# Kernel optimization log

Hardware: AMD Instinct MI355X
Metric: run time of the kernel (lower is better)

Reference implementation:

```python
import jax, jax.numpy as jnp
import numpy as np

SEARCH_RANGE = 4  # matches args.search_range


def _displacements(r):
    # Exact channel ordering of the original double loop:
    # I=0 -> (0,0); then for i=1..r: (-i,0),(+i,0),(0,-i),(0,+i),
    # then for j=1..r: (-i,-j),(+i,+j),(-i,+j),(+i,-j).
    ds = [(0, 0)]
    for i in range(1, r + 1):
        ds += [(-i, 0), (i, 0), (0, -i), (0, i)]
        for j in range(1, r + 1):
            ds += [(-i, -j), (i, j), (-i, j), (i, -j)]
    return ds


def setup_inputs() -> dict:
    key = jax.random.key(0)
    k1, k2 = jax.random.split(key)
    B, C, H, W = 4, 128, 96, 160
    src = jax.random.normal(k1, (B, C, H, W), dtype=jnp.float32)
    tgt = jax.random.normal(k2, (B, C, H, W), dtype=jnp.float32)
    return {"src": src, "tgt": tgt}


def reference(src, tgt):
    r = SEARCH_RANGE
    B, C, H, W = src.shape
    D = (2 * r + 1) ** 2  # 81 displacement channels
    # Zero-pad tgt spatially so out-of-range shifted regions contribute 0,
    # matching the torch version's zero-initialized output slices.
    tgt_pad = jnp.pad(tgt, ((0, 0), (0, 0), (r, r), (r, r)))
    chans = []
    for dy, dx in _displacements(r):
        # shifted[b,c,y,x] = tgt[b,c,y+dy,x+dx] (0 outside)
        t = jax.lax.dynamic_slice(tgt_pad, (0, 0, r + dy, r + dx), (B, C, H, W))
        chans.append(jnp.einsum('bchw,bchw->bhw', src, t))
    out = jnp.stack(chans, axis=1)  # [B, D, H, W]
    return out / D
```

## Files before the change

kernel.cpp:

```cpp
#include <hip/hip_runtime.h>
#include <hip/hip_bf16.h>

#define BATCH 4
#define CHAN 128
#define HGT 96
#define WID 160
#define HW (HGT * WID)
#define THREADS 256
#define TENSOR_ELEMS (BATCH * CHAN * HGT * WID)
#define WS_NEED ((size_t)(2 * (size_t)TENSOR_ELEMS * 2))

typedef __attribute__((ext_vector_type(8))) short short8;
typedef __attribute__((ext_vector_type(4))) float float4v;

__device__ __forceinline__ int chan_of(int dy, int dx) {
    if (dy == 0 && dx == 0) return 0;
    if (dx == 0) { int i = dy < 0 ? -dy : dy; return 1 + (i - 1) * 20 + (dy < 0 ? 0 : 1); }
    if (dy == 0) { int i = dx < 0 ? -dx : dx; return 1 + (i - 1) * 20 + (dx < 0 ? 2 : 3); }
    int i = dy < 0 ? -dy : dy;
    int j = dx < 0 ? -dx : dx;
    int s = (dy < 0) ? (dx < 0 ? 0 : 2) : (dx < 0 ? 3 : 1);
    return 1 + (i - 1) * 20 + 4 + (j - 1) * 4 + s;
}

__device__ __forceinline__ unsigned pk2(float a, float b) {
    __hip_bfloat162 h = __float22bfloat162_rn(make_float2(a, b));
    unsigned u;
    __builtin_memcpy(&u, &h, 4);
    return u;
}

union sl_u { uint4 v; short8 s; };

__global__ __launch_bounds__(THREADS)
void nhwc_bf16_kernel(const float* __restrict__ src,
                      const float* __restrict__ tgt,
                      ushort* __restrict__ ws) {
    __shared__ unsigned s_t[64][65];
    int r = blockIdx.x;
    const int xb = r % 3; r /= 3;
    const int y  = r % HGT; r /= HGT;
    const int b  = r % BATCH; r /= BATCH;
    const float* in = r ? tgt : src;
    ushort* op0 = ws + (size_t)r * TENSOR_ELEMS;
    const int x0 = xb * 64;
    const int npx = (x0 + 64 <= WID) ? 64 : (WID - x0);

    const int t  = threadIdx.x;
    const int x1 = t & 63, cp0 = t >> 6;
    if (x1 < npx) {
        const int base = (b * CHAN * HGT + y) * WID + x0 + x1;
        #pragma unroll
        for (int i = 0; i < 16; ++i) {
            const int cp = cp0 + i * 4;
            float a = in[base + (2 * cp) * HW];
            float c = in[base + (2 * cp + 1) * HW];
            s_t[cp][x1] = pk2(a, c);
        }
    }
    __syncthreads();
    const int x2 = t >> 2, g = t & 3;
    if (x2 < npx) {
        ushort* op = op0 + ((size_t)(b * HGT + y) * WID + x0 + x2) * CHAN + g * 32;
        #pragma unroll
        for (int k = 0; k < 4; ++k) {
            uint4 v;
            v.x = s_t[g * 16 + k * 4 + 0][x2];
            v.y = s_t[g * 16 + k * 4 + 1][x2];
            v.z = s_t[g * 16 + k * 4 + 2][x2];
            v.w = s_t[g * 16 + k * 4 + 3][x2];
            *(uint4*)(op + k * 8) = v;
        }
    }
}

__global__ __launch_bounds__(THREADS)
void cost_volume_mfma(const ushort* __restrict__ srcT,
                      const ushort* __restrict__ tgtT,
                      float* __restrict__ out) {
    __shared__ __align__(16) uint4 s_b[2432];
    __shared__ int s_tab[27];

    const int tid  = threadIdx.x;
    const int wv   = tid >> 6;
    const int lane = tid & 63;
    const int q    = lane >> 4;
    const int ln   = lane & 15;

    const int w    = blockIdx.x;
    const int slab = w & 7;
    const int b    = slab >> 1;
    const int yh   = slab & 1;
    const int r0   = w >> 3;
    const int dyg  = r0 % 3;
    const int t    = r0 / 3;
    const int x0   = (t % 10) * 16;
    const int y0   = yh * 48 + (t / 10) * 4;
    const int dy0  = dyg * 3 - 4;

    if (tid < 27) s_tab[tid] = chan_of(dy0 + tid / 9, tid % 9 - 4) * HW;

    const ushort* tbase = tgtT + (size_t)b * HGT * WID * CHAN;
    #pragma unroll
    for (int k = 0; k < 9; ++k) {
        const int u   = k * THREADS + tid;
        const int j   = u & 15;
        const int v16 = u >> 4;
        const int row = v16 / 24;
        const int x   = v16 - row * 24;
        const int gr  = y0 + dy0 + row;
        const int gx  = x0 - 4 + x;
        const int oct = j ^ (x & 15);
        unsigned* lp = (unsigned*)&s_b[k * THREADS + (tid & ~63)];
        if (((unsigned)gr < (unsigned)HGT) && ((unsigned)gx < (unsigned)WID)) {
            const unsigned* gp =
                (const unsigned*)(tbase + ((gr * WID + gx) * CHAN + oct * 8));
            __builtin_amdgcn_global_load_lds(gp, lp, 16, 0, 0);
        } else {
            s_b[u] = make_uint4(0u, 0u, 0u, 0u);
        }
    }

    const int y = y0 + wv;
    const ushort* abase =
        srcT + ((size_t)(b * HGT + y) * WID + x0 + ln) * CHAN + q * 8;
    short8 afr[4];
    #pragma unroll
    for (int ks = 0; ks < 4; ++ks)
        afr[ks] = *(const short8*)(abase + ks * 32);

    __syncthreads();

    const float inv = 1.0f / 81.0f;
    const int obase = (b * 81 * HGT + y) * WID + x0;
    #pragma unroll
    for (int dyi = 0; dyi < 3; ++dyi) {
        const int rr = wv + dyi;
        float4v a0 = (float4v){0.f, 0.f, 0.f, 0.f};
        float4v a1 = (float4v){0.f, 0.f, 0.f, 0.f};
        #pragma unroll
        for (int ks = 0; ks < 4; ++ks) {
            sl_u b0;
            b0.v = s_b[(rr * 24 + ln) * 16 + ((q + ks * 4) ^ ln)];
            a0 = __builtin_amdgcn_mfma_f32_16x16x32_bf16(afr[ks], b0.s, a0, 0, 0, 0);
        }
        #pragma unroll
        for (int ks = 0; ks < 4; ++ks) {
            sl_u b1;
            b1.v = s_b[(rr * 24 + 16 + ln) * 16 + ((q + ks * 4) ^ ln)];
            a1 = __builtin_amdgcn_mfma_f32_16x16x32_bf16(afr[ks], b1.s, a1, 0, 0, 0);
        }
        #pragma unroll
        for (int reg = 0; reg < 4; ++reg) {
            const int m = q * 4 + reg;
            const int t0x = ln - m;
            if ((unsigned)t0x <= 8u)
                out[obase + s_tab[dyi * 9 + t0x] + m] = a0[reg] * inv;
            const int t1x = ln + 16 - m;
            if ((unsigned)t1x <= 8u)
                out[obase + s_tab[dyi * 9 + t1x] + m] = a1[reg] * inv;
        }
    }
}

#define ST_DECODE(TAG, U)                                                     \
    const int oct##TAG = (U) & 15;                                            \
    const int u4##TAG  = (U) >> 4;                                            \
    const int row##TAG = (u4##TAG * 43) >> 8;                                 \
    const int xq##TAG  = u4##TAG - row##TAG * 6;                              \
    const int gr##TAG  = y0 + dy0 + row##TAG;                                 \
    const int gx##TAG  = x0 - 4 + xq##TAG * 4;                                \
    const bool ok##TAG = ((unsigned)gr##TAG < (unsigned)HGT) &&               \
                         ((unsigned)gx##TAG < (unsigned)WID);                 \
    const int ga##TAG  = tb + (oct##TAG * 8 * HGT + gr##TAG) * WID + gx##TAG;

#define ST_ISSUE(TAG, COND)                                                   \
    _Pragma("unroll")                                                         \
    for (int j = 0; j < 8; ++j)                                               \
        p##TAG[j] = (COND) ? *(const float4v*)(tgt + ga##TAG + j * HW)        \
                           : (float4v){0.f, 0.f, 0.f, 0.f};

#define ST_WRITE(TAG)                                                         \
    _Pragma("unroll")                                                         \
    for (int i = 0; i < 4; ++i) {                                             \
        const int xl = xq##TAG * 4 + i;                                       \
        uint4 val;                                                            \
        val.x = pk2(p##TAG[0][i], p##TAG[1][i]);                              \
        val.y = pk2(p##TAG[2][i], p##TAG[3][i]);                              \
        val.z = pk2(p##TAG[4][i], p##TAG[5][i]);                              \
        val.w = pk2(p##TAG[6][i], p##TAG[7][i]);                              \
        s_b[(row##TAG * 24 + xl) * 16 + (oct##TAG ^ (xl & 15))] = val;        \
    }

__global__ __launch_bounds__(THREADS, 4)
void cost_volume_fallback(const float* __restrict__ src,
                          const float* __restrict__ tgt,
                          float* __restrict__ out) {
    __shared__ __align__(16) uint4 s_b[2432];
    __shared__ int s_tab[27];

    const int tid  = threadIdx.x;
    const int wv   = tid >> 6;
    const int lane = tid & 63;
    const int q    = lane >> 4;
    const int ln   = lane & 15;

    const int w    = blockIdx.x;
    const int slab = w & 7;
    const int b    = slab >> 1;
    const int yh   = slab & 1;
    const int r0   = w >> 3;
    const int dyg  = r0 % 3;
    const int t    = r0 / 3;
    const int x0   = (t % 10) * 16;
    const int y0   = yh * 48 + (t / 10) * 4;
    const int dy0  = dyg * 3 - 4;

    if (tid < 27) s_tab[tid] = chan_of(dy0 + tid / 9, tid % 9 - 4) * HW;

    const int tb = b * CHAN * HGT * WID;

    ST_DECODE(0, tid)
    ST_DECODE(1, tid + 256)
    ST_DECODE(2, tid + 512)
    const bool has2 = tid < 64;

    float4v p0[8], p1[8], p2[8];
    ST_ISSUE(0, ok0)

    const int y  = y0 + wv;
    const int sbase = (b * CHAN * HGT + y) * WID + x0 + ln + q * 8 * HW;
    float apay[32];
    #pragma unroll
    for (int ks = 0; ks < 4; ++ks)
        #pragma unroll
        for (int j = 0; j < 8; ++j)
            apay[ks * 8 + j] = src[sbase + (ks * 32 + j) * HW];

    ST_ISSUE(1, ok1)
    ST_WRITE(0)
    ST_ISSUE(2, has2 && ok2)
    short8 afr[4];
    #pragma unroll
    for (int ks = 0; ks < 4; ++ks) {
        sl_u f;
        f.v.x = pk2(apay[ks * 8 + 0], apay[ks * 8 + 1]);
        f.v.y = pk2(apay[ks * 8 + 2], apay[ks * 8 + 3]);
        f.v.z = pk2(apay[ks * 8 + 4], apay[ks * 8 + 5]);
        f.v.w = pk2(apay[ks * 8 + 6], apay[ks * 8 + 7]);
        afr[ks] = f.s;
    }
    ST_WRITE(1)
    if (has2) { ST_WRITE(2) }

    __syncthreads();

    const float inv = 1.0f / 81.0f;
    const int obase = (b * 81 * HGT + y) * WID + x0;
    #pragma unroll
    for (int dyi = 0; dyi < 3; ++dyi) {
        const int rr = wv + dyi;
        float4v a0 = (float4v){0.f, 0.f, 0.f, 0.f};
        float4v a1 = (float4v){0.f, 0.f, 0.f, 0.f};
        #pragma unroll
        for (int ks = 0; ks < 4; ++ks) {
            sl_u b0;
            b0.v = s_b[(rr * 24 + ln) * 16 + ((q + ks * 4) ^ ln)];
            a0 = __builtin_amdgcn_mfma_f32_16x16x32_bf16(afr[ks], b0.s, a0, 0, 0, 0);
        }
        #pragma unroll
        for (int ks = 0; ks < 4; ++ks) {
            sl_u b1;
            b1.v = s_b[(rr * 24 + 16 + ln) * 16 + ((q + ks * 4) ^ ln)];
            a1 = __builtin_amdgcn_mfma_f32_16x16x32_bf16(afr[ks], b1.s, a1, 0, 0, 0);
        }
        #pragma unroll
        for (int reg = 0; reg < 4; ++reg) {
            const int m = q * 4 + reg;
            const int t0x = ln - m;
            if ((unsigned)t0x <= 8u)
                out[obase + s_tab[dyi * 9 + t0x] + m] = a0[reg] * inv;
            const int t1x = ln + 16 - m;
            if ((unsigned)t1x <= 8u)
                out[obase + s_tab[dyi * 9 + t1x] + m] = a1[reg] * inv;
        }
    }
}

extern "C" void kernel_launch(void* const* d_in, const int* in_sizes, int n_in,
                              void* d_out, int out_size, void* d_ws, size_t ws_size,
                              hipStream_t stream) {
    const float* src = (const float*)d_in[0];
    const float* tgt = (const float*)d_in[1];
    float* out = (float*)d_out;
    if (d_ws && ws_size >= WS_NEED) {
        ushort* ws = (ushort*)d_ws;
        nhwc_bf16_kernel<<<dim3(2304, 1, 1), dim3(THREADS, 1, 1), 0, stream>>>(src, tgt, ws);
        cost_volume_mfma<<<dim3(2880, 1, 1), dim3(THREADS, 1, 1), 0, stream>>>(
            ws, ws + TENSOR_ELEMS, out);
    } else {
        cost_volume_fallback<<<dim3(2880, 1, 1), dim3(THREADS, 1, 1), 0, stream>>>(src, tgt, out);
    }
}
```

Before: 120.2 us.

## Read src directly in fp32, transpose only tgt, stage outputs through LDS

The prepass now converts only tgt to NHWC bf16. The main kernel loads its src A-fragments straight from the fp32 NCHW input and packs them to bf16 in registers, which removes the src write/read round trip through workspace. MFMA results are staged in shared memory, so each channel's 4x16 tile goes out as coalesced float4 stores instead of scattered scalar writes. Launch bounds now request 4 blocks per CU. The costs are more registers (32 floats per thread), an extra barrier, and strided fp32 src loads.

```diff
diff --git a/kernel.cpp b/kernel.cpp
--- a/kernel.cpp
+++ b/kernel.cpp
@@ -8,7 +8,7 @@
 #define HW (HGT * WID)
 #define THREADS 256
 #define TENSOR_ELEMS (BATCH * CHAN * HGT * WID)
-#define WS_NEED ((size_t)(2 * (size_t)TENSOR_ELEMS * 2))
+#define WS_NEED ((size_t)TENSOR_ELEMS * 2)
 
 typedef __attribute__((ext_vector_type(8))) short short8;
 typedef __attribute__((ext_vector_type(4))) float float4v;
@@ -33,16 +33,12 @@
 union sl_u { uint4 v; short8 s; };
 
 __global__ __launch_bounds__(THREADS)
-void nhwc_bf16_kernel(const float* __restrict__ src,
-                      const float* __restrict__ tgt,
-                      ushort* __restrict__ ws) {
+void nhwc_bf16_tgt(const float* __restrict__ tgt, ushort* __restrict__ ws) {
     __shared__ unsigned s_t[64][65];
     int r = blockIdx.x;
     const int xb = r % 3; r /= 3;
     const int y  = r % HGT; r /= HGT;
-    const int b  = r % BATCH; r /= BATCH;
-    const float* in = r ? tgt : src;
-    ushort* op0 = ws + (size_t)r * TENSOR_ELEMS;
+    const int b  = r;
     const int x0 = xb * 64;
     const int npx = (x0 + 64 <= WID) ? 64 : (WID - x0);
 
@@ -53,15 +49,14 @@
         #pragma unroll
         for (int i = 0; i < 16; ++i) {
             const int cp = cp0 + i * 4;
-            float a = in[base + (2 * cp) * HW];
-            float c = in[base + (2 * cp + 1) * HW];
-            s_t[cp][x1] = pk2(a, c);
+            s_t[cp][x1] = pk2(tgt[base + (2 * cp) * HW],
+                              tgt[base + (2 * cp + 1) * HW]);
         }
     }
     __syncthreads();
     const int x2 = t >> 2, g = t & 3;
     if (x2 < npx) {
-        ushort* op = op0 + ((size_t)(b * HGT + y) * WID + x0 + x2) * CHAN + g * 32;
+        ushort* op = ws + ((size_t)(b * HGT + y) * WID + x0 + x2) * CHAN + g * 32;
         #pragma unroll
         for (int k = 0; k < 4; ++k) {
             uint4 v;
@@ -74,8 +69,8 @@
     }
 }
 
-__global__ __launch_bounds__(THREADS)
-void cost_volume_mfma(const ushort* __restrict__ srcT,
+__global__ __launch_bounds__(THREADS, 4)
+void cost_volume_mfma(const float* __restrict__ src,
                       const ushort* __restrict__ tgtT,
                       float* __restrict__ out) {
     __shared__ __align__(16) uint4 s_b[2432];
@@ -99,6 +94,15 @@
     const int dy0  = dyg * 3 - 4;
 
     if (tid < 27) s_tab[tid] = chan_of(dy0 + tid / 9, tid % 9 - 4) * HW;
+
+    const int y = y0 + wv;
+    const int sbase = (b * CHAN * HGT + y) * WID + x0 + ln + q * 8 * HW;
+    float apay[32];
+    #pragma unroll
+    for (int ks = 0; ks < 4; ++ks)
+        #pragma unroll
+        for (int j = 0; j < 8; ++j)
+            apay[ks * 8 + j] = src[sbase + (ks * 32 + j) * HW];
 
     const ushort* tbase = tgtT + (size_t)b * HGT * WID * CHAN;
     #pragma unroll
@@ -121,18 +125,20 @@
         }
     }
 
-    const int y = y0 + wv;
-    const ushort* abase =
-        srcT + ((size_t)(b * HGT + y) * WID + x0 + ln) * CHAN + q * 8;
     short8 afr[4];
     #pragma unroll
-    for (int ks = 0; ks < 4; ++ks)
-        afr[ks] = *(const short8*)(abase + ks * 32);
-
-    __syncthreads();
-
-    const float inv = 1.0f / 81.0f;
-    const int obase = (b * 81 * HGT + y) * WID + x0;
+    for (int ks = 0; ks < 4; ++ks) {
+        sl_u f;
+        f.v.x = pk2(apay[ks * 8 + 0], apay[ks * 8 + 1]);
+        f.v.y = pk2(apay[ks * 8 + 2], apay[ks * 8 + 3]);
+        f.v.z = pk2(apay[ks * 8 + 4], apay[ks * 8 + 5]);
+        f.v.w = pk2(apay[ks * 8 + 6], apay[ks * 8 + 7]);
+        afr[ks] = f.s;
+    }
+
+    __syncthreads();
+
+    float4v aa0[3], aa1[3];
     #pragma unroll
     for (int dyi = 0; dyi < 3; ++dyi) {
         const int rr = wv + dyi;
@@ -150,15 +156,40 @@
             b1.v = s_b[(rr * 24 + 16 + ln) * 16 + ((q + ks * 4) ^ ln)];
             a1 = __builtin_amdgcn_mfma_f32_16x16x32_bf16(afr[ks], b1.s, a1, 0, 0, 0);
         }
+        aa0[dyi] = a0;
+        aa1[dyi] = a1;
+    }
+
+    __syncthreads();
+
+    float* s_o = (float*)s_b;
+    const float inv = 1.0f / 81.0f;
+    #pragma unroll
+    for (int dyi = 0; dyi < 3; ++dyi) {
         #pragma unroll
         for (int reg = 0; reg < 4; ++reg) {
             const int m = q * 4 + reg;
             const int t0x = ln - m;
             if ((unsigned)t0x <= 8u)
-                out[obase + s_tab[dyi * 9 + t0x] + m] = a0[reg] * inv;
+                s_o[(dyi * 9 + t0x) * 68 + wv * 16 + m] = aa0[dyi][reg] * inv;
             const int t1x = ln + 16 - m;
             if ((unsigned)t1x <= 8u)
-                out[obase + s_tab[dyi * 9 + t1x] + m] = a1[reg] * inv;
+                s_o[(dyi * 9 + t1x) * 68 + wv * 16 + m] = aa1[dyi][reg] * inv;
+        }
+    }
+    __syncthreads();
+
+    const size_t ob = (size_t)b * 81 * HW + (size_t)y0 * WID + x0;
+    #pragma unroll
+    for (int it = 0; it < 2; ++it) {
+        const int v = it * THREADS + tid;
+        if (v < 432) {
+            const int xq  = v & 3;
+            const int row = v >> 2;
+            const int cix = row >> 2;
+            const int yy  = row & 3;
+            float4v val = *(const float4v*)&s_o[cix * 68 + yy * 16 + xq * 4];
+            *(float4v*)&out[ob + s_tab[cix] + yy * WID + xq * 4] = val;
         }
     }
 }
@@ -295,9 +326,8 @@
     float* out = (float*)d_out;
     if (d_ws && ws_size >= WS_NEED) {
         ushort* ws = (ushort*)d_ws;
-        nhwc_bf16_kernel<<<dim3(2304, 1, 1), dim3(THREADS, 1, 1), 0, stream>>>(src, tgt, ws);
-        cost_volume_mfma<<<dim3(2880, 1, 1), dim3(THREADS, 1, 1), 0, stream>>>(
-            ws, ws + TENSOR_ELEMS, out);
+        nhwc_bf16_tgt<<<dim3(1152, 1, 1), dim3(THREADS, 1, 1), 0, stream>>>(tgt, ws);
+        cost_volume_mfma<<<dim3(2880, 1, 1), dim3(THREADS, 1, 1), 0, stream>>>(src, ws, out);
     } else {
         cost_volume_fallback<<<dim3(2880, 1, 1), dim3(THREADS, 1, 1), 0, stream>>>(src, tgt, out);
     }
```

Measured after the change: 123.2 us. 1.02x slower.
